# Performance work log

Measured on AMD Instinct MI355X. Metric: run time of the kernel, lower is better.

The kernel has to match this reference:

```python
import jax, jax.numpy as jnp
import numpy as np

INV_SQRT2 = 0.7071067811865476  # Haar (db1) filter coefficient


def _haar_wavedec(x, level):
    """Haar (db1) multi-level DWT along axis=2 of x: [B,H,L,Dh].
    Returns [cA_n, cD_n, cD_{n-1}, ..., cD_1] (pywt.wavedec ordering).
    Exact match to pywt for L divisible by 2**level (no boundary padding needed)."""
    details = []
    a = x
    for _ in range(level):
        e, o = a[:, :, 0::2, :], a[:, :, 1::2, :]
        details.append((e - o) * INV_SQRT2)
        a = (e + o) * INV_SQRT2
    return [a] + details[::-1]


def _haar_idwt_step(a, d):
    """Single-level Haar inverse DWT along axis=2."""
    e = (a + d) * INV_SQRT2
    o = (a - d) * INV_SQRT2
    B, H, Lh, Dh = a.shape
    return jnp.stack([e, o], axis=3).reshape(B, H, 2 * Lh, Dh)


def setup_inputs() -> dict:
    key = jax.random.key(0)
    ks = jax.random.split(key, 6)
    B, L, D, H, M = 8, 4096, 1024, 16, 3
    Dh = D // H
    return {
        "query": jax.random.normal(ks[0], (B, L, D), jnp.float32),
        "W_qkv": jax.random.normal(ks[1], (3 * D, D), jnp.float32) * 0.02,
        "b_qkv": jnp.zeros((3 * D,), jnp.float32),
        "W_out": jax.random.normal(ks[2], (D, D), jnp.float32) * 0.02,
        "b_out": jnp.zeros((D,), jnp.float32),
        "weight_q": jax.random.normal(ks[3], (H, M, Dh), jnp.float32),
        "weight_v": jax.random.normal(ks[4], (H, M, Dh), jnp.float32),
    }


def reference(query, W_qkv, b_qkv, W_out, b_out, weight_q, weight_v):
    B, L, D = query.shape
    H, M, Dh = weight_q.shape  # n_heads, modes, head_dim

    qkv = query @ W_qkv.T + b_qkv               # [B,L,3D]; k chunk is unused (as in original)
    q = qkv[..., :D].reshape(B, L, H, Dh).transpose(0, 2, 1, 3)      # [B,H,L,Dh]
    v = qkv[..., 2 * D:].reshape(B, L, H, Dh).transpose(0, 2, 1, 3)  # [B,H,L,Dh]

    cq = _haar_wavedec(q, M)  # [cA_M, cD_M, ..., cD_1]
    cv = _haar_wavedec(v, M)

    # Weight the coarsest `modes` bands per head/channel, then multiply q*v in wavelet domain.
    prod = []
    for j in range(M):
        wq = weight_q[None, :, j, None, :]  # [1,H,1,Dh]
        wv = weight_v[None, :, j, None, :]
        prod.append((cq[j] * wq) * (cv[j] * wv))
    prod.append(cq[M] * cv[M])  # finest detail band, unweighted

    # Inverse DWT back to length L.
    a = prod[0]
    for d in prod[1:]:
        a = _haar_idwt_step(a, d)

    out = a.transpose(0, 2, 1, 3).reshape(B, L, D)
    return out @ W_out.T + b_out  # dropout is identity in eval
```

## Files before the change

### kernel.cpp

```cpp
#include <hip/hip_runtime.h>
#include <hip/hip_fp16.h>
#include <cstdint>
#include <cstddef>

typedef _Float16 f16;
typedef __attribute__((ext_vector_type(4))) _Float16 f16x4;
typedef __attribute__((ext_vector_type(8))) _Float16 f16x8;
typedef __attribute__((ext_vector_type(4))) float f32x4;

#define C_INV_SQRT2 0.70710678118654752440f

__device__ __forceinline__ void gld_lds16(const void* g, void* l) {
  __builtin_amdgcn_global_load_lds((const __attribute__((address_space(1))) void*)g,
                                   (__attribute__((address_space(3))) void*)l, 16, 0, 0);
}

__global__ __launch_bounds__(256) void cvt_f32_f16_k(const float* __restrict__ in,
                                                     f16* __restrict__ out, int n4) {
  int i = blockIdx.x * 256 + threadIdx.x;
  if (i >= n4) return;
  const float4 x = ((const float4*)in)[i];
  f16x4 y;
  y.x = (f16)x.x; y.y = (f16)x.y; y.z = (f16)x.z; y.w = (f16)x.w;
  ((f16x4*)out)[i] = y;
}

__global__ __launch_bounds__(256) void pack_wqv_k(const float* __restrict__ W,
                                                  const float* __restrict__ b,
                                                  f16* __restrict__ Wo,
                                                  float* __restrict__ bo) {
  int i = blockIdx.x * 256 + threadIdx.x;
  int n = i >> 8;
  int c = (i & 255) * 4;
  int sn = (n < 1024) ? n : (n + 1024);
  const float4 x = *(const float4*)(W + (size_t)sn * 1024 + c);
  f16x4 y; y.x = (f16)x.x; y.y = (f16)x.y; y.z = (f16)x.z; y.w = (f16)x.w;
  *(f16x4*)(Wo + (size_t)n * 1024 + c) = y;
  if (i < 2048) bo[i] = b[(i < 1024) ? i : (i + 1024)];
}


#define STAGE(bufidx, k0)                                                          \
  {                                                                                \
    f16* LA = &lds[bufidx][0][0];                                                  \
    f16* LB = &lds[bufidx][1][0];                                                  \
    _Pragma("unroll") for (int i = 0; i < 4; i++) {                                \
      const int u = i * 512 + t;                                                   \
      const int row = u >> 3;                                                      \
      const int col = ((u & 7) ^ (row & 7)) << 3;                                  \
      gld_lds16(GA + (size_t)row * K + (k0) + col, LA + (i * 512 + (w << 6)) * 8); \
    }                                                                              \
    _Pragma("unroll") for (int i = 0; i < 4; i++) {                                \
      const int u = i * 512 + t;                                                   \
      const int row = u >> 3;                                                      \
      const int col = ((u & 7) ^ (row & 7)) << 3;                                  \
      gld_lds16(GB + (size_t)row * K + (k0) + col, LB + (i * 512 + (w << 6)) * 8); \
    }                                                                              \
  }

#define COMPUTE(bufidx)                                                            \
  {                                                                                \
    const f16* As_ = &lds[bufidx][0][0];                                           \
    const f16* Bs_ = &lds[bufidx][1][0];                                           \
    const f16* pA0 = As_ + wm * 4096 + lb0;                                        \
    const f16* pA1 = As_ + wm * 4096 + lb1;                                        \
    const f16* pB0 = Bs_ + wn * 8192 + lb0;                                        \
    const f16* pB1 = Bs_ + wn * 8192 + lb1;                                        \
    f16x8 af[4][2];                                                                \
    _Pragma("unroll") for (int mi = 0; mi < 4; mi++) {                             \
      af[mi][0] = *(const f16x8*)(pA0 + mi * 1024);                                \
      af[mi][1] = *(const f16x8*)(pA1 + mi * 1024);                                \
    }                                                                              \
    _Pragma("unroll") for (int nh = 0; nh < 2; nh++) {                             \
      f16x8 bf[4][2];                                                              \
      _Pragma("unroll") for (int nj = 0; nj < 4; nj++) {                           \
        bf[nj][0] = *(const f16x8*)(pB0 + (nh * 4 + nj) * 1024);                   \
        bf[nj][1] = *(const f16x8*)(pB1 + (nh * 4 + nj) * 1024);                   \
      }                                                                            \
      __builtin_amdgcn_s_setprio(1);                                               \
      _Pragma("unroll") for (int mi = 0; mi < 4; mi++)                             \
        _Pragma("unroll") for (int nj = 0; nj < 4; nj++) {                         \
          acc[mi][nh * 4 + nj] = __builtin_amdgcn_mfma_f32_16x16x32_f16(           \
              af[mi][0], bf[nj][0], acc[mi][nh * 4 + nj], 0, 0, 0);                \
          acc[mi][nh * 4 + nj] = __builtin_amdgcn_mfma_f32_16x16x32_f16(           \
              af[mi][1], bf[nj][1], acc[mi][nh * 4 + nj], 0, 0, 0);                \
        }                                                                          \
      __builtin_amdgcn_s_setprio(0);                                               \
    }                                                                              \
  }

template <typename CT>
__global__ __launch_bounds__(512, 2) void gemm256_k(const f16* __restrict__ A,
                                                    const f16* __restrict__ B,
                                                    const float* __restrict__ bias,
                                                    CT* __restrict__ C,
                                                    int M, int N, int K, int nbx) {
  __shared__ f16 lds[2][2][256 * 64];
  const int t = threadIdx.x;
  const int w = t >> 6, l = t & 63;
  const int wm = w >> 1, wn = w & 1;
  const int hi = l >> 4, lo = l & 15;

  const int nwg = gridDim.x;
  const int cpx = nwg >> 3;
  const int bid = blockIdx.x;
  const int nid = (bid & 7) * cpx + (bid >> 3);
  const int by = nid / nbx, bx = nid - by * nbx;
  const int m0 = by * 256, n0 = bx * 256;

  const f16* GA = A + (size_t)m0 * K;
  const f16* GB = B + (size_t)n0 * K;

  const int lb0 = lo * 64 + ((hi ^ (l & 7)) << 3);
  const int lb1 = lo * 64 + (((4 | hi) ^ (l & 7)) << 3);

  f32x4 acc[4][8] = {};
  const int NT = K >> 6;

  STAGE(0, 0);
  for (int tt = 0; tt < NT - 1; ++tt) {
    const int cur = tt & 1;
    STAGE(cur ^ 1, (tt + 1) << 6);
    asm volatile("s_waitcnt vmcnt(8)" ::: "memory");
    __builtin_amdgcn_s_barrier();
    __builtin_amdgcn_sched_barrier(0);
    COMPUTE(cur);
    __builtin_amdgcn_sched_barrier(0);
    __builtin_amdgcn_s_barrier();
  }
  asm volatile("s_waitcnt vmcnt(0)" ::: "memory");
  __builtin_amdgcn_s_barrier();
  __builtin_amdgcn_sched_barrier(0);
  COMPUTE((NT - 1) & 1);

#pragma unroll
  for (int mi = 0; mi < 4; mi++) {
#pragma unroll
    for (int nj = 0; nj < 8; nj++) {
      const int col = n0 + wn * 128 + nj * 16 + lo;
      const float bb = bias[col];
      const size_t base = (size_t)(m0 + wm * 64 + mi * 16 + hi * 4) * N + col;
#pragma unroll
      for (int r = 0; r < 4; r++) C[base + (size_t)r * N] = (CT)(acc[mi][nj][r] + bb);
    }
  }
}

__global__ __launch_bounds__(256) void dwt_middle_k(const f16* __restrict__ qv,
                                                    const float* __restrict__ wq,
                                                    const float* __restrict__ wv,
                                                    f16* __restrict__ out) {
  const int idx = blockIdx.x * 256 + threadIdx.x;
  const int d = idx & 1023;
  const int g = idx >> 10;
  const size_t m0 = (size_t)g * 8;
  const int h = d >> 6, dh = d & 63;

  float q[8], v[8];
#pragma unroll
  for (int i = 0; i < 8; i++) {
    q[i] = (float)qv[(m0 + i) * 2048 + d];
    v[i] = (float)qv[(m0 + i) * 2048 + 1024 + d];
  }
  const float c = C_INV_SQRT2;
  float qa1[4], qd1[4], va1[4], vd1[4];
#pragma unroll
  for (int i = 0; i < 4; i++) {
    qd1[i] = (q[2 * i] - q[2 * i + 1]) * c;
    qa1[i] = (q[2 * i] + q[2 * i + 1]) * c;
    vd1[i] = (v[2 * i] - v[2 * i + 1]) * c;
    va1[i] = (v[2 * i] + v[2 * i + 1]) * c;
  }
  float qa2[2], qd2[2], va2[2], vd2[2];
#pragma unroll
  for (int j = 0; j < 2; j++) {
    qd2[j] = (qa1[2 * j] - qa1[2 * j + 1]) * c;
    qa2[j] = (qa1[2 * j] + qa1[2 * j + 1]) * c;
    vd2[j] = (va1[2 * j] - va1[2 * j + 1]) * c;
    va2[j] = (va1[2 * j] + va1[2 * j + 1]) * c;
  }
  const float qd3 = (qa2[0] - qa2[1]) * c, qa3 = (qa2[0] + qa2[1]) * c;
  const float vd3 = (va2[0] - va2[1]) * c, va3 = (va2[0] + va2[1]) * c;

  const int wb = h * 192 + dh;
  const float wq0 = wq[wb], wq1 = wq[wb + 64], wq2 = wq[wb + 128];
  const float wv0 = wv[wb], wv1 = wv[wb + 64], wv2 = wv[wb + 128];

  const float pa = (qa3 * wq0) * (va3 * wv0);
  const float pd3 = (qd3 * wq1) * (vd3 * wv1);
  float pd2[2], pd1[4];
#pragma unroll
  for (int j = 0; j < 2; j++) pd2[j] = (qd2[j] * wq2) * (vd2[j] * wv2);
#pragma unroll
  for (int i = 0; i < 4; i++) pd1[i] = qd1[i] * vd1[i];

  float s2[2], s1[4], a8[8];
  s2[0] = (pa + pd3) * c;
  s2[1] = (pa - pd3) * c;
#pragma unroll
  for (int j = 0; j < 2; j++) {
    s1[2 * j] = (s2[j] + pd2[j]) * c;
    s1[2 * j + 1] = (s2[j] - pd2[j]) * c;
  }
#pragma unroll
  for (int i = 0; i < 4; i++) {
    a8[2 * i] = (s1[i] + pd1[i]) * c;
    a8[2 * i + 1] = (s1[i] - pd1[i]) * c;
  }
#pragma unroll
  for (int i = 0; i < 8; i++) out[(m0 + i) * 1024 + d] = (f16)a8[i];
}

extern "C" void kernel_launch(void* const* d_in, const int* in_sizes, int n_in,
                              void* d_out, int out_size, void* d_ws, size_t ws_size,
                              hipStream_t stream) {
  (void)in_sizes; (void)n_in; (void)out_size; (void)ws_size;
  const float* query = (const float*)d_in[0];
  const float* W_qkv = (const float*)d_in[1];
  const float* b_qkv = (const float*)d_in[2];
  const float* W_out = (const float*)d_in[3];
  const float* b_out = (const float*)d_in[4];
  const float* wq = (const float*)d_in[5];
  const float* wv = (const float*)d_in[6];
  float* out = (float*)d_out;

  char* ws = (char*)d_ws;
  f16* qf16 = (f16*)ws;
  f16* Wqv = (f16*)(ws + 67108864);
  float* bqv = (float*)(ws + 67108864 + 4194304);
  f16* Wout = (f16*)(ws + 67108864 + 4194304 + 8192);
  f16* qv = (f16*)d_out;
  f16* a_f16 = qf16;

  cvt_f32_f16_k<<<dim3(8388608 / 256), dim3(256), 0, stream>>>(query, qf16, 8388608);
  pack_wqv_k<<<dim3(2048), dim3(256), 0, stream>>>(W_qkv, b_qkv, Wqv, bqv);
  cvt_f32_f16_k<<<dim3(262144 / 256), dim3(256), 0, stream>>>(W_out, Wout, 262144);
  gemm256_k<f16><<<dim3((2048 / 256) * (32768 / 256)), dim3(512), 0, stream>>>(
      qf16, Wqv, bqv, qv, 32768, 2048, 1024, 2048 / 256);
  dwt_middle_k<<<dim3(16384), dim3(256), 0, stream>>>(qv, wq, wv, a_f16);
  gemm256_k<float><<<dim3((1024 / 256) * (32768 / 256)), dim3(512), 0, stream>>>(
      a_f16, Wout, b_out, out, 32768, 1024, 1024, 1024 / 256);
}
```

Baseline: 290.9 us.

## Use 4-stage K=32 pipeline with 2x4 warp grid and vectorize DWT kernel

The GEMM moves from a double-buffered K=64 tile to a four-deep ring of K=32 stages, with three stages prefetched ahead and matching vmcnt waits. The warp layout changes from 4x2 to 2x4, so each warp computes 128x64 with 8x4 accumulators, and LDS fragment offsets are precomputed with a new swizzle. The DWT kernel now processes four channels per thread using f16x4 vector loads and stores, cutting the thread count fourfold. The deeper pipeline is meant to hide global-load latency, but it brings more barriers per K step and new swizzle logic that could introduce bank conflicts or errors.

```diff
diff --git a/kernel.cpp b/kernel.cpp
--- a/kernel.cpp
+++ b/kernel.cpp
@@ -40,53 +40,14 @@
 }
 
 
-#define STAGE(bufidx, k0)                                                          \
-  {                                                                                \
-    f16* LA = &lds[bufidx][0][0];                                                  \
-    f16* LB = &lds[bufidx][1][0];                                                  \
-    _Pragma("unroll") for (int i = 0; i < 4; i++) {                                \
-      const int u = i * 512 + t;                                                   \
-      const int row = u >> 3;                                                      \
-      const int col = ((u & 7) ^ (row & 7)) << 3;                                  \
-      gld_lds16(GA + (size_t)row * K + (k0) + col, LA + (i * 512 + (w << 6)) * 8); \
-    }                                                                              \
-    _Pragma("unroll") for (int i = 0; i < 4; i++) {                                \
-      const int u = i * 512 + t;                                                   \
-      const int row = u >> 3;                                                      \
-      const int col = ((u & 7) ^ (row & 7)) << 3;                                  \
-      gld_lds16(GB + (size_t)row * K + (k0) + col, LB + (i * 512 + (w << 6)) * 8); \
-    }                                                                              \
-  }
-
-#define COMPUTE(bufidx)                                                            \
-  {                                                                                \
-    const f16* As_ = &lds[bufidx][0][0];                                           \
-    const f16* Bs_ = &lds[bufidx][1][0];                                           \
-    const f16* pA0 = As_ + wm * 4096 + lb0;                                        \
-    const f16* pA1 = As_ + wm * 4096 + lb1;                                        \
-    const f16* pB0 = Bs_ + wn * 8192 + lb0;                                        \
-    const f16* pB1 = Bs_ + wn * 8192 + lb1;                                        \
-    f16x8 af[4][2];                                                                \
-    _Pragma("unroll") for (int mi = 0; mi < 4; mi++) {                             \
-      af[mi][0] = *(const f16x8*)(pA0 + mi * 1024);                                \
-      af[mi][1] = *(const f16x8*)(pA1 + mi * 1024);                                \
-    }                                                                              \
-    _Pragma("unroll") for (int nh = 0; nh < 2; nh++) {                             \
-      f16x8 bf[4][2];                                                              \
-      _Pragma("unroll") for (int nj = 0; nj < 4; nj++) {                           \
-        bf[nj][0] = *(const f16x8*)(pB0 + (nh * 4 + nj) * 1024);                   \
-        bf[nj][1] = *(const f16x8*)(pB1 + (nh * 4 + nj) * 1024);                   \
-      }                                                                            \
-      __builtin_amdgcn_s_setprio(1);                                               \
-      _Pragma("unroll") for (int mi = 0; mi < 4; mi++)                             \
-        _Pragma("unroll") for (int nj = 0; nj < 4; nj++) {                         \
-          acc[mi][nh * 4 + nj] = __builtin_amdgcn_mfma_f32_16x16x32_f16(           \
-              af[mi][0], bf[nj][0], acc[mi][nh * 4 + nj], 0, 0, 0);                \
-          acc[mi][nh * 4 + nj] = __builtin_amdgcn_mfma_f32_16x16x32_f16(           \
-              af[mi][1], bf[nj][1], acc[mi][nh * 4 + nj], 0, 0, 0);                \
-        }                                                                          \
-      __builtin_amdgcn_s_setprio(0);                                               \
-    }                                                                              \
+#define STAGE4(bufi, k0)                          \
+  {                                               \
+    f16* LA = &lds[bufi][0][0];                   \
+    f16* LB = &lds[bufi][1][0];                   \
+    gld_lds16(pGA0 + (k0), LA + dst0);            \
+    gld_lds16(pGA1 + (k0), LA + dst1);            \
+    gld_lds16(pGB0 + (k0), LB + dst0);            \
+    gld_lds16(pGB1 + (k0), LB + dst1);            \
   }
 
 template <typename CT>
@@ -95,10 +56,10 @@
                                                     const float* __restrict__ bias,
                                                     CT* __restrict__ C,
                                                     int M, int N, int K, int nbx) {
-  __shared__ f16 lds[2][2][256 * 64];
+  __shared__ f16 lds[4][2][256 * 32];
   const int t = threadIdx.x;
   const int w = t >> 6, l = t & 63;
-  const int wm = w >> 1, wn = w & 1;
+  const int wm = w >> 2, wn = w & 3;
   const int hi = l >> 4, lo = l & 15;
 
   const int nwg = gridDim.x;
@@ -111,35 +72,79 @@
   const f16* GA = A + (size_t)m0 * K;
   const f16* GB = B + (size_t)n0 * K;
 
-  const int lb0 = lo * 64 + ((hi ^ (l & 7)) << 3);
-  const int lb1 = lo * 64 + (((4 | hi) ^ (l & 7)) << 3);
-
-  f32x4 acc[4][8] = {};
-  const int NT = K >> 6;
-
-  STAGE(0, 0);
-  for (int tt = 0; tt < NT - 1; ++tt) {
-    const int cur = tt & 1;
-    STAGE(cur ^ 1, (tt + 1) << 6);
-    asm volatile("s_waitcnt vmcnt(8)" ::: "memory");
+  int rowS[2], chS[2];
+#pragma unroll
+  for (int i = 0; i < 2; i++) {
+    const int u = i * 512 + t;
+    rowS[i] = u >> 2;
+    chS[i] = (u & 3) ^ ((u >> 3) & 3);
+  }
+  const f16* pGA0 = GA + (size_t)rowS[0] * K + chS[0] * 8;
+  const f16* pGA1 = GA + (size_t)rowS[1] * K + chS[1] * 8;
+  const f16* pGB0 = GB + (size_t)rowS[0] * K + chS[0] * 8;
+  const f16* pGB1 = GB + (size_t)rowS[1] * K + chS[1] * 8;
+  const int dst0 = (0 * 512 + w * 64) * 8;
+  const int dst1 = (1 * 512 + w * 64) * 8;
+
+  int offA[8], offB[4];
+#pragma unroll
+  for (int mi = 0; mi < 8; mi++) {
+    const int r = wm * 128 + mi * 16 + lo;
+    offA[mi] = r * 32 + ((hi ^ ((r >> 1) & 3)) << 3);
+  }
+#pragma unroll
+  for (int nj = 0; nj < 4; nj++) {
+    const int r = wn * 64 + nj * 16 + lo;
+    offB[nj] = r * 32 + ((hi ^ ((r >> 1) & 3)) << 3);
+  }
+
+  f32x4 acc[8][4] = {};
+  const int NS = K >> 5;
+
+  STAGE4(0, 0);
+  STAGE4(1, 32);
+  STAGE4(2, 64);
+
+  for (int s = 0; s < NS; ++s) {
+    const int cur = s & 3;
+    if (s < NS - 3) {
+      STAGE4((s + 3) & 3, (s + 3) * 32);
+      asm volatile("s_waitcnt vmcnt(12)" ::: "memory");
+    } else if (s == NS - 3) {
+      asm volatile("s_waitcnt vmcnt(8)" ::: "memory");
+    } else if (s == NS - 2) {
+      asm volatile("s_waitcnt vmcnt(4)" ::: "memory");
+    } else {
+      asm volatile("s_waitcnt vmcnt(0)" ::: "memory");
+    }
     __builtin_amdgcn_s_barrier();
     __builtin_amdgcn_sched_barrier(0);
-    COMPUTE(cur);
+    const f16* pA = &lds[cur][0][0];
+    const f16* pB = &lds[cur][1][0];
+    f16x8 af[8], bf[4];
+#pragma unroll
+    for (int mi = 0; mi < 8; mi++) af[mi] = *(const f16x8*)(pA + offA[mi]);
+#pragma unroll
+    for (int nj = 0; nj < 4; nj++) bf[nj] = *(const f16x8*)(pB + offB[nj]);
+    __builtin_amdgcn_s_setprio(1);
+#pragma unroll
+    for (int mi = 0; mi < 8; mi++)
+#pragma unroll
+      for (int nj = 0; nj < 4; nj++)
+        acc[mi][nj] =
+            __builtin_amdgcn_mfma_f32_16x16x32_f16(af[mi], bf[nj], acc[mi][nj], 0, 0, 0);
+    __builtin_amdgcn_s_setprio(0);
     __builtin_amdgcn_sched_barrier(0);
     __builtin_amdgcn_s_barrier();
   }
-  asm volatile("s_waitcnt vmcnt(0)" ::: "memory");
-  __builtin_amdgcn_s_barrier();
-  __builtin_amdgcn_sched_barrier(0);
-  COMPUTE((NT - 1) & 1);
-
-#pragma unroll
-  for (int mi = 0; mi < 4; mi++) {
-#pragma unroll
-    for (int nj = 0; nj < 8; nj++) {
-      const int col = n0 + wn * 128 + nj * 16 + lo;
+
+#pragma unroll
+  for (int mi = 0; mi < 8; mi++) {
+#pragma unroll
+    for (int nj = 0; nj < 4; nj++) {
+      const int col = n0 + wn * 64 + nj * 16 + lo;
       const float bb = bias[col];
-      const size_t base = (size_t)(m0 + wm * 64 + mi * 16 + hi * 4) * N + col;
+      const size_t base = (size_t)(m0 + wm * 128 + mi * 16 + hi * 4) * N + col;
 #pragma unroll
       for (int r = 0; r < 4; r++) C[base + (size_t)r * N] = (CT)(acc[mi][nj][r] + bb);
     }
@@ -150,65 +155,72 @@
                                                     const float* __restrict__ wq,
                                                     const float* __restrict__ wv,
                                                     f16* __restrict__ out) {
-  const int idx = blockIdx.x * 256 + threadIdx.x;
-  const int d = idx & 1023;
-  const int g = idx >> 10;
+  const int g = blockIdx.x;
+  const int d0 = threadIdx.x * 4;
   const size_t m0 = (size_t)g * 8;
-  const int h = d >> 6, dh = d & 63;
-
-  float q[8], v[8];
+
+  f16x4 qr[8], vr[8], o[8];
 #pragma unroll
   for (int i = 0; i < 8; i++) {
-    q[i] = (float)qv[(m0 + i) * 2048 + d];
-    v[i] = (float)qv[(m0 + i) * 2048 + 1024 + d];
+    qr[i] = *(const f16x4*)(qv + (m0 + i) * 2048 + d0);
+    vr[i] = *(const f16x4*)(qv + (m0 + i) * 2048 + 1024 + d0);
   }
   const float c = C_INV_SQRT2;
-  float qa1[4], qd1[4], va1[4], vd1[4];
-#pragma unroll
-  for (int i = 0; i < 4; i++) {
-    qd1[i] = (q[2 * i] - q[2 * i + 1]) * c;
-    qa1[i] = (q[2 * i] + q[2 * i + 1]) * c;
-    vd1[i] = (v[2 * i] - v[2 * i + 1]) * c;
-    va1[i] = (v[2 * i] + v[2 * i + 1]) * c;
-  }
-  float qa2[2], qd2[2], va2[2], vd2[2];
-#pragma unroll
-  for (int j = 0; j < 2; j++) {
-    qd2[j] = (qa1[2 * j] - qa1[2 * j + 1]) * c;
-    qa2[j] = (qa1[2 * j] + qa1[2 * j + 1]) * c;
-    vd2[j] = (va1[2 * j] - va1[2 * j + 1]) * c;
-    va2[j] = (va1[2 * j] + va1[2 * j + 1]) * c;
-  }
-  const float qd3 = (qa2[0] - qa2[1]) * c, qa3 = (qa2[0] + qa2[1]) * c;
-  const float vd3 = (va2[0] - va2[1]) * c, va3 = (va2[0] + va2[1]) * c;
-
-  const int wb = h * 192 + dh;
-  const float wq0 = wq[wb], wq1 = wq[wb + 64], wq2 = wq[wb + 128];
-  const float wv0 = wv[wb], wv1 = wv[wb + 64], wv2 = wv[wb + 128];
-
-  const float pa = (qa3 * wq0) * (va3 * wv0);
-  const float pd3 = (qd3 * wq1) * (vd3 * wv1);
-  float pd2[2], pd1[4];
-#pragma unroll
-  for (int j = 0; j < 2; j++) pd2[j] = (qd2[j] * wq2) * (vd2[j] * wv2);
-#pragma unroll
-  for (int i = 0; i < 4; i++) pd1[i] = qd1[i] * vd1[i];
-
-  float s2[2], s1[4], a8[8];
-  s2[0] = (pa + pd3) * c;
-  s2[1] = (pa - pd3) * c;
-#pragma unroll
-  for (int j = 0; j < 2; j++) {
-    s1[2 * j] = (s2[j] + pd2[j]) * c;
-    s1[2 * j + 1] = (s2[j] - pd2[j]) * c;
-  }
-#pragma unroll
-  for (int i = 0; i < 4; i++) {
-    a8[2 * i] = (s1[i] + pd1[i]) * c;
-    a8[2 * i + 1] = (s1[i] - pd1[i]) * c;
-  }
-#pragma unroll
-  for (int i = 0; i < 8; i++) out[(m0 + i) * 1024 + d] = (f16)a8[i];
+#pragma unroll
+  for (int dd = 0; dd < 4; dd++) {
+    const int d = d0 + dd;
+    const int h = d >> 6, dh = d & 63;
+    float q[8], v[8];
+#pragma unroll
+    for (int i = 0; i < 8; i++) { q[i] = (float)qr[i][dd]; v[i] = (float)vr[i][dd]; }
+
+    float qa1[4], qd1[4], va1[4], vd1[4];
+#pragma unroll
+    for (int i = 0; i < 4; i++) {
+      qd1[i] = (q[2 * i] - q[2 * i + 1]) * c;
+      qa1[i] = (q[2 * i] + q[2 * i + 1]) * c;
+      vd1[i] = (v[2 * i] - v[2 * i + 1]) * c;
+      va1[i] = (v[2 * i] + v[2 * i + 1]) * c;
+    }
+    float qa2[2], qd2[2], va2[2], vd2[2];
+#pragma unroll
+    for (int j = 0; j < 2; j++) {
+      qd2[j] = (qa1[2 * j] - qa1[2 * j + 1]) * c;
+      qa2[j] = (qa1[2 * j] + qa1[2 * j + 1]) * c;
+      vd2[j] = (va1[2 * j] - va1[2 * j + 1]) * c;
+      va2[j] = (va1[2 * j] + va1[2 * j + 1]) * c;
+    }
+    const float qd3 = (qa2[0] - qa2[1]) * c, qa3 = (qa2[0] + qa2[1]) * c;
+    const float vd3 = (va2[0] - va2[1]) * c, va3 = (va2[0] + va2[1]) * c;
+
+    const int wb = h * 192 + dh;
+    const float wq0 = wq[wb], wq1 = wq[wb + 64], wq2 = wq[wb + 128];
+    const float wv0 = wv[wb], wv1 = wv[wb + 64], wv2 = wv[wb + 128];
+
+    const float pa = (qa3 * wq0) * (va3 * wv0);
+    const float pd3 = (qd3 * wq1) * (vd3 * wv1);
+    float pd2[2], pd1[4];
+#pragma unroll
+    for (int j = 0; j < 2; j++) pd2[j] = (qd2[j] * wq2) * (vd2[j] * wv2);
+#pragma unroll
+    for (int i = 0; i < 4; i++) pd1[i] = qd1[i] * vd1[i];
+
+    float s2[2], s1[4];
+    s2[0] = (pa + pd3) * c;
+    s2[1] = (pa - pd3) * c;
+#pragma unroll
+    for (int j = 0; j < 2; j++) {
+      s1[2 * j] = (s2[j] + pd2[j]) * c;
+      s1[2 * j + 1] = (s2[j] - pd2[j]) * c;
+    }
+#pragma unroll
+    for (int i = 0; i < 4; i++) {
+      o[2 * i][dd] = (f16)((s1[i] + pd1[i]) * c);
+      o[2 * i + 1][dd] = (f16)((s1[i] - pd1[i]) * c);
+    }
+  }
+#pragma unroll
+  for (int i = 0; i < 8; i++) *(f16x4*)(out + (m0 + i) * 1024 + d0) = o[i];
 }
 
 extern "C" void kernel_launch(void* const* d_in, const int* in_sizes, int n_in,
@@ -237,7 +249,7 @@
   cvt_f32_f16_k<<<dim3(262144 / 256), dim3(256), 0, stream>>>(W_out, Wout, 262144);
   gemm256_k<f16><<<dim3((2048 / 256) * (32768 / 256)), dim3(512), 0, stream>>>(
       qf16, Wqv, bqv, qv, 32768, 2048, 1024, 2048 / 256);
-  dwt_middle_k<<<dim3(16384), dim3(256), 0, stream>>>(qv, wq, wv, a_f16);
+  dwt_middle_k<<<dim3(4096), dim3(256), 0, stream>>>(qv, wq, wv, a_f16);
   gemm256_k<float><<<dim3((1024 / 256) * (32768 / 256)), dim3(512), 0, stream>>>(
       a_f16, Wout, b_out, out, 32768, 1024, 1024, 1024 / 256);
 }
```

Result: slower. 305.5 us (+5.0%).
